# Kernel optimization log

Measured on AMD Instinct MI355X. Metric: run time of the kernel, lower is better.

The kernel has to match this reference:

```python
import jax, jax.numpy as jnp
import numpy as np

N_NODES = 50000
N_EDGES = 800000
IN_CH = 128
HID = 64
OUT_CH = 2
NEG_SLOPE = 0.2


def gcn_conv(x, src, dst, deg_isqrt, W, b):
    # PyG GCNConv: x @ W, symmetric normalization with self-loops, scatter-add, + bias
    h = x @ W  # [N, HID]
    norm = deg_isqrt[src] * deg_isqrt[dst]  # [E+N]
    msg = h[src] * norm[:, None]  # gather + scale
    out = jax.ops.segment_sum(msg, dst, num_segments=x.shape[0])
    return out + b


def setup_inputs() -> dict:
    key = jax.random.key(0)
    ks = jax.random.split(key, 16)
    glorot = lambda k, i, o: jax.random.normal(k, (i, o), jnp.float32) * jnp.sqrt(2.0 / (i + o))
    inp = {
        "node_features": jax.random.normal(ks[0], (N_NODES, IN_CH), jnp.float32),
        "edge_index": jax.random.randint(ks[1], (2, N_EDGES), 0, N_NODES, jnp.int64 if jax.config.jax_enable_x64 else jnp.int32),
        "fc1_W": glorot(ks[2], IN_CH, 32), "fc1_b": jnp.zeros((32,), jnp.float32),
        "fc2_W": glorot(ks[3], 32, HID), "fc2_b": jnp.zeros((HID,), jnp.float32),
        "conv1_W": glorot(ks[4], HID, HID), "conv1_b": jnp.zeros((HID,), jnp.float32),
        "conv2_W": glorot(ks[5], HID, HID), "conv2_b": jnp.zeros((HID,), jnp.float32),
        "conv3_W": glorot(ks[6], HID, HID), "conv3_b": jnp.zeros((HID,), jnp.float32),
        "conv4_W": glorot(ks[7], HID, HID), "conv4_b": jnp.zeros((HID,), jnp.float32),
        "final_W": glorot(ks[8], HID, OUT_CH), "final_b": jnp.zeros((OUT_CH,), jnp.float32),
    }
    return inp


def reference(node_features, edge_index, fc1_W, fc1_b, fc2_W, fc2_b,
              conv1_W, conv1_b, conv2_W, conv2_b, conv3_W, conv3_b,
              conv4_W, conv4_b, final_W, final_b):
    N = node_features.shape[0]
    # add self-loops once (shared by all conv layers)
    loops = jnp.arange(N, dtype=edge_index.dtype)
    src = jnp.concatenate([edge_index[0], loops])
    dst = jnp.concatenate([edge_index[1], loops])
    deg = jax.ops.segment_sum(jnp.ones_like(dst, jnp.float32), dst, num_segments=N)
    deg_isqrt = jnp.where(deg > 0, jax.lax.rsqrt(jnp.maximum(deg, 1.0)), 0.0)

    lrelu = lambda x: jnp.where(x >= 0, x, NEG_SLOPE * x)

    x = jax.nn.relu(node_features @ fc1_W + fc1_b) @ fc2_W + fc2_b  # fc stack
    out1 = lrelu(gcn_conv(x, src, dst, deg_isqrt, conv1_W, conv1_b))
    out2 = lrelu(gcn_conv(out1, src, dst, deg_isqrt, conv2_W, conv2_b)) + out1
    out3 = lrelu(gcn_conv(out2, src, dst, deg_isqrt, conv3_W, conv3_b))
    out4 = gcn_conv(out3, src, dst, deg_isqrt, conv4_W, conv4_b) + out2
    return out4 @ final_W + final_b
```

## Files before the change

### kernel.cpp

```cpp
#include <hip/hip_runtime.h>

#define NN 50000
#define NE 800000

typedef unsigned short u16;
typedef unsigned int u32;

__device__ inline float rlf(float v, int l) {
    return __int_as_float(__builtin_amdgcn_readlane(__float_as_int(v), l));
}
__device__ inline u16 f2bf(float f) {
    u32 u = __float_as_uint(f);
    u32 r = (u + 0x7FFFu + ((u >> 16) & 1u)) >> 16;
    return (u16)r;
}
__device__ inline float lo16(u32 q) { return __uint_as_float(q << 16); }
__device__ inline float hi16(u32 q) { return __uint_as_float(q & 0xffff0000u); }

__global__ void k_hist(const int* __restrict__ dst, int* __restrict__ cnt) {
    int e = blockIdx.x * 256 + threadIdx.x;
    if (e < NE) atomicAdd(&cnt[dst[e]], 1);
}

__global__ void k_disq(const int* __restrict__ cnt, float* __restrict__ disq) {
    int i = blockIdx.x * 256 + threadIdx.x;
    if (i < NN) disq[i] = rsqrtf((float)cnt[i] + 1.0f);
}

__global__ __launch_bounds__(1024) void k_scan(int* __restrict__ cnt,
                                               int* __restrict__ rowptr) {
    __shared__ int wsum[16];
    __shared__ int carry;
    int t = threadIdx.x, wave = t >> 6, lane = t & 63;
    if (t == 0) { carry = 0; rowptr[0] = 0; }
    __syncthreads();
    for (int base = 0; base < NN; base += 1024) {
        int i = base + t;
        int x = (i < NN) ? cnt[i] : 0;
        if (i < NN) cnt[i] = 0;
        for (int off = 1; off < 64; off <<= 1) {
            int y = __shfl_up(x, off, 64);
            if (lane >= off) x += y;
        }
        if (lane == 63) wsum[wave] = x;
        __syncthreads();
        if (wave == 0 && lane < 16) {
            int w = wsum[lane];
            for (int off = 1; off < 16; off <<= 1) {
                int y = __shfl_up(w, off, 16);
                if (lane >= off) w += y;
            }
            wsum[lane] = w;
        }
        __syncthreads();
        int incl = carry + ((wave > 0) ? wsum[wave - 1] : 0) + x;
        if (i < NN) rowptr[i + 1] = incl;
        __syncthreads();
        if (t == 1023) carry = incl;
        __syncthreads();
    }
}

__global__ void k_fill(const int* __restrict__ src, const int* __restrict__ dst,
                       const int* __restrict__ rowptr, int* __restrict__ cur,
                       int* __restrict__ esrc) {
    int e = blockIdx.x * 256 + threadIdx.x;
    if (e < NE) {
        int d = dst[e];
        int pos = rowptr[d] + atomicAdd(&cur[d], 1);
        esrc[pos] = src[e];
    }
}

__global__ __launch_bounds__(64) void k_foldw(
    const float* __restrict__ fc2W, const float* __restrict__ b2,
    const float* __restrict__ c1W, float* __restrict__ W2c,
    float* __restrict__ b2c) {
    int c = threadIdx.x;
    int j = blockIdx.x;
    float s = 0.f;
    if (j < 32) {
        for (int k = 0; k < 64; ++k) s = fmaf(fc2W[j * 64 + k], c1W[k * 64 + c], s);
        W2c[j * 64 + c] = s;
    } else {
        for (int k = 0; k < 64; ++k) s = fmaf(b2[k], c1W[k * 64 + c], s);
        b2c[c] = s;
    }
}

__global__ __launch_bounds__(256) void k_fc(
    const float* __restrict__ nf,
    const float* __restrict__ W1, const float* __restrict__ b1,
    const float* __restrict__ W2c, const float* __restrict__ b2c,
    const float* __restrict__ disq, u16* __restrict__ Hb) {
    int lane = threadIdx.x & 63;
    int c = lane & 31, h = lane >> 5;
    int wid = (blockIdx.x * 256 + threadIdx.x) >> 6;
    int nwaves = (gridDim.x * 256) >> 6;
    float w1[64], w2[32];
    #pragma unroll
    for (int j = 0; j < 64; ++j) w1[j] = W1[(h * 64 + j) * 32 + c];
    #pragma unroll
    for (int j = 0; j < 32; ++j) w2[j] = W2c[j * 64 + lane];
    float b1c = b1[c], b2l = b2c[lane];
    for (int n = wid; n < NN; n += nwaves) {
        float x0 = nf[(size_t)n * 128 + lane];
        float x1 = nf[(size_t)n * 128 + 64 + lane];
        float s = 0.f;
        #pragma unroll
        for (int j = 0; j < 64; ++j) {
            float xa = rlf(x0, j), xb = rlf(x1, j);
            s = fmaf(h ? xb : xa, w1[j], s);
        }
        s += __shfl_xor(s, 32, 64);
        float hv = fmaxf(s + b1c, 0.f);
        float o = b2l;
        #pragma unroll
        for (int j = 0; j < 32; ++j) o = fmaf(rlf(hv, j), w2[j], o);
        Hb[(size_t)n * 64 + lane] = f2bf(disq[n] * o);
    }
}

__global__ __launch_bounds__(256) void k_gemm64(
    const float* __restrict__ X, const float* __restrict__ W,
    const float* __restrict__ disq, u16* __restrict__ Hb) {
    int lane = threadIdx.x & 63;
    int wid = (blockIdx.x * 256 + threadIdx.x) >> 6;
    int nwaves = (gridDim.x * 256) >> 6;
    float wcol[64];
    #pragma unroll
    for (int k = 0; k < 64; ++k) wcol[k] = W[k * 64 + lane];
    for (int n = wid; n < NN; n += nwaves) {
        float xv = X[(size_t)n * 64 + lane];
        float acc = 0.f;
        #pragma unroll
        for (int k = 0; k < 64; ++k) acc = fmaf(rlf(xv, k), wcol[k], acc);
        Hb[(size_t)n * 64 + lane] = f2bf(disq[n] * acc);
    }
}

__global__ __launch_bounds__(256) void k_csr_conv(
    const u16* __restrict__ Hb, const int* __restrict__ rowptr,
    const int* __restrict__ esrc, const float* __restrict__ disq,
    const float* __restrict__ b, const float* __restrict__ res,
    float* __restrict__ out, int do_lrelu) {
    int lane = threadIdx.x & 63;
    int half = lane >> 5;
    int cl = (lane & 31) * 2;
    int n = (blockIdx.x * 256 + threadIdx.x) >> 6;
    if (n >= NN) return;
    int beg = rowptr[n], end = rowptr[n + 1];
    float a0 = 0.f, a1 = 0.f;
    for (int base = beg; base < end; base += 64) {
        int cnt = min(64, end - base);
        int idx = (lane < cnt) ? esrc[base + lane] : 0;
        int j = 0;
        for (; j + 8 <= cnt; j += 8) {
            int p0 = __builtin_amdgcn_readlane(idx, j + 0);
            int p1 = __builtin_amdgcn_readlane(idx, j + 1);
            int p2 = __builtin_amdgcn_readlane(idx, j + 2);
            int p3 = __builtin_amdgcn_readlane(idx, j + 3);
            int p4 = __builtin_amdgcn_readlane(idx, j + 4);
            int p5 = __builtin_amdgcn_readlane(idx, j + 5);
            int p6 = __builtin_amdgcn_readlane(idx, j + 6);
            int p7 = __builtin_amdgcn_readlane(idx, j + 7);
            int sA = half ? p1 : p0;
            int sB = half ? p3 : p2;
            int sC = half ? p5 : p4;
            int sD = half ? p7 : p6;
            u32 qA = *(const u32*)(Hb + ((size_t)sA * 64 + cl));
            u32 qB = *(const u32*)(Hb + ((size_t)sB * 64 + cl));
            u32 qC = *(const u32*)(Hb + ((size_t)sC * 64 + cl));
            u32 qD = *(const u32*)(Hb + ((size_t)sD * 64 + cl));
            a0 += (lo16(qA) + lo16(qB)) + (lo16(qC) + lo16(qD));
            a1 += (hi16(qA) + hi16(qB)) + (hi16(qC) + hi16(qD));
        }
        for (; j + 2 <= cnt; j += 2) {
            int p0 = __builtin_amdgcn_readlane(idx, j);
            int p1 = __builtin_amdgcn_readlane(idx, j + 1);
            int s = half ? p1 : p0;
            u32 q = *(const u32*)(Hb + ((size_t)s * 64 + cl));
            a0 += lo16(q);
            a1 += hi16(q);
        }
        if (j < cnt) {
            int s = __builtin_amdgcn_readlane(idx, j);
            if (!half) {
                u32 q = *(const u32*)(Hb + ((size_t)s * 64 + cl));
                a0 += lo16(q);
                a1 += hi16(q);
            }
        }
    }
    a0 += __shfl_xor(a0, 32, 64);
    a1 += __shfl_xor(a1, 32, 64);
    u32 qs = *(const u32*)(Hb + ((size_t)n * 64 + cl));
    a0 += lo16(qs);
    a1 += hi16(qs);
    float dn = disq[n];
    float v0 = dn * a0 + b[cl];
    float v1 = dn * a1 + b[cl + 1];
    if (do_lrelu) {
        v0 = (v0 >= 0.f) ? v0 : 0.2f * v0;
        v1 = (v1 >= 0.f) ? v1 : 0.2f * v1;
    }
    if (res) {
        float2 r = *(const float2*)(res + ((size_t)n * 64 + cl));
        v0 += r.x;
        v1 += r.y;
    }
    if (!half) {
        float2 o;
        o.x = v0;
        o.y = v1;
        *(float2*)(out + ((size_t)n * 64 + cl)) = o;
    }
}

__global__ __launch_bounds__(256) void k_csr_conv_final(
    const u16* __restrict__ Hb, const int* __restrict__ rowptr,
    const int* __restrict__ esrc, const float* __restrict__ disq,
    const float* __restrict__ b, const float* __restrict__ res,
    const float* __restrict__ FW, const float* __restrict__ fb,
    float* __restrict__ out) {
    int lane = threadIdx.x & 63;
    int half = lane >> 5;
    int cl = (lane & 31) * 2;
    int n = (blockIdx.x * 256 + threadIdx.x) >> 6;
    if (n >= NN) return;
    int beg = rowptr[n], end = rowptr[n + 1];
    float a0 = 0.f, a1 = 0.f;
    for (int base = beg; base < end; base += 64) {
        int cnt = min(64, end - base);
        int idx = (lane < cnt) ? esrc[base + lane] : 0;
        int j = 0;
        for (; j + 8 <= cnt; j += 8) {
            int p0 = __builtin_amdgcn_readlane(idx, j + 0);
            int p1 = __builtin_amdgcn_readlane(idx, j + 1);
            int p2 = __builtin_amdgcn_readlane(idx, j + 2);
            int p3 = __builtin_amdgcn_readlane(idx, j + 3);
            int p4 = __builtin_amdgcn_readlane(idx, j + 4);
            int p5 = __builtin_amdgcn_readlane(idx, j + 5);
            int p6 = __builtin_amdgcn_readlane(idx, j + 6);
            int p7 = __builtin_amdgcn_readlane(idx, j + 7);
            int sA = half ? p1 : p0;
            int sB = half ? p3 : p2;
            int sC = half ? p5 : p4;
            int sD = half ? p7 : p6;
            u32 qA = *(const u32*)(Hb + ((size_t)sA * 64 + cl));
            u32 qB = *(const u32*)(Hb + ((size_t)sB * 64 + cl));
            u32 qC = *(const u32*)(Hb + ((size_t)sC * 64 + cl));
            u32 qD = *(const u32*)(Hb + ((size_t)sD * 64 + cl));
            a0 += (lo16(qA) + lo16(qB)) + (lo16(qC) + lo16(qD));
            a1 += (hi16(qA) + hi16(qB)) + (hi16(qC) + hi16(qD));
        }
        for (; j + 2 <= cnt; j += 2) {
            int p0 = __builtin_amdgcn_readlane(idx, j);
            int p1 = __builtin_amdgcn_readlane(idx, j + 1);
            int s = half ? p1 : p0;
            u32 q = *(const u32*)(Hb + ((size_t)s * 64 + cl));
            a0 += lo16(q);
            a1 += hi16(q);
        }
        if (j < cnt) {
            int s = __builtin_amdgcn_readlane(idx, j);
            if (!half) {
                u32 q = *(const u32*)(Hb + ((size_t)s * 64 + cl));
                a0 += lo16(q);
                a1 += hi16(q);
            }
        }
    }
    a0 += __shfl_xor(a0, 32, 64);
    a1 += __shfl_xor(a1, 32, 64);
    u32 qs = *(const u32*)(Hb + ((size_t)n * 64 + cl));
    a0 += lo16(qs);
    a1 += hi16(qs);
    float dn = disq[n];
    float2 r = *(const float2*)(res + ((size_t)n * 64 + cl));
    float v0 = dn * a0 + b[cl] + r.x;
    float v1 = dn * a1 + b[cl + 1] + r.y;
    float p0 = v0 * FW[cl * 2 + 0] + v1 * FW[(cl + 1) * 2 + 0];
    float p1 = v0 * FW[cl * 2 + 1] + v1 * FW[(cl + 1) * 2 + 1];
    for (int off = 16; off; off >>= 1) {
        p0 += __shfl_xor(p0, off, 64);
        p1 += __shfl_xor(p1, off, 64);
    }
    if (lane == 0) {
        out[n * 2 + 0] = p0 + fb[0];
        out[n * 2 + 1] = p1 + fb[1];
    }
}

extern "C" void kernel_launch(void* const* d_in, const int* in_sizes, int n_in,
                              void* d_out, int out_size, void* d_ws, size_t ws_size,
                              hipStream_t stream) {
    const float* nf   = (const float*)d_in[0];
    const int*   ei   = (const int*)d_in[1];
    const float* fc1W = (const float*)d_in[2];
    const float* fc1b = (const float*)d_in[3];
    const float* fc2W = (const float*)d_in[4];
    const float* fc2b = (const float*)d_in[5];
    const float* cW[4] = {(const float*)d_in[6], (const float*)d_in[8],
                          (const float*)d_in[10], (const float*)d_in[12]};
    const float* cb[4] = {(const float*)d_in[7], (const float*)d_in[9],
                          (const float*)d_in[11], (const float*)d_in[13]};
    const float* fW = (const float*)d_in[14];
    const float* fb = (const float*)d_in[15];
    const int* src = ei;
    const int* dst = ei + NE;

    float* ws     = (float*)d_ws;
    float* disq   = ws;
    int*   cnt    = (int*)(ws + 50048);
    int*   rowptr = cnt + 50048;
    int*   esrc   = rowptr + 50056;
    float* W2c    = (float*)(esrc + 800000);
    float* b2c    = W2c + 2048;
    float* B0     = b2c + 64;
    float* B1     = B0 + (size_t)NN * 64;
    u16*   Hb     = (u16*)(B1 + (size_t)NN * 64);

    hipMemsetAsync(cnt, 0, 50048 * sizeof(int), stream);
    k_hist<<<(NE + 255) / 256, 256, 0, stream>>>(dst, cnt);
    k_disq<<<(NN + 255) / 256, 256, 0, stream>>>(cnt, disq);
    k_scan<<<1, 1024, 0, stream>>>(cnt, rowptr);
    k_fill<<<(NE + 255) / 256, 256, 0, stream>>>(src, dst, rowptr, cnt, esrc);

    k_foldw<<<33, 64, 0, stream>>>(fc2W, fc2b, cW[0], W2c, b2c);
    k_fc<<<1024, 256, 0, stream>>>(nf, fc1W, fc1b, W2c, b2c, disq, Hb);

    const int cgrid = (NN * 64 + 255) / 256;

    k_csr_conv<<<cgrid, 256, 0, stream>>>(Hb, rowptr, esrc, disq, cb[0], nullptr, B1, 1);
    k_gemm64<<<512, 256, 0, stream>>>(B1, cW[1], disq, Hb);
    k_csr_conv<<<cgrid, 256, 0, stream>>>(Hb, rowptr, esrc, disq, cb[1], B1, B0, 1);
    k_gemm64<<<512, 256, 0, stream>>>(B0, cW[2], disq, Hb);
    k_csr_conv<<<cgrid, 256, 0, stream>>>(Hb, rowptr, esrc, disq, cb[2], nullptr, B1, 1);
    k_gemm64<<<512, 256, 0, stream>>>(B1, cW[3], disq, Hb);
    k_csr_conv_final<<<cgrid, 256, 0, stream>>>(Hb, rowptr, esrc, disq, cb[3], B0,
                                                fW, fb, (float*)d_out);
}
```

Before: 356.6 us.

## Fuse preprocessing launches and store CSR source indices as 16-bit

```diff
diff --git a/kernel.cpp b/kernel.cpp
--- a/kernel.cpp
+++ b/kernel.cpp
@@ -2,6 +2,9 @@
 
 #define NN 50000
 #define NE 800000
+#define HIST_BLOCKS ((NE + 255) / 256)
+#define FILL_BLOCKS HIST_BLOCKS
+#define FC_BLOCKS 1024
 
 typedef unsigned short u16;
 typedef unsigned int u32;
@@ -17,18 +20,32 @@
 __device__ inline float lo16(u32 q) { return __uint_as_float(q << 16); }
 __device__ inline float hi16(u32 q) { return __uint_as_float(q & 0xffff0000u); }
 
-__global__ void k_hist(const int* __restrict__ dst, int* __restrict__ cnt) {
-    int e = blockIdx.x * 256 + threadIdx.x;
-    if (e < NE) atomicAdd(&cnt[dst[e]], 1);
-}
-
-__global__ void k_disq(const int* __restrict__ cnt, float* __restrict__ disq) {
-    int i = blockIdx.x * 256 + threadIdx.x;
-    if (i < NN) disq[i] = rsqrtf((float)cnt[i] + 1.0f);
+__global__ __launch_bounds__(256) void k_hist_foldw(
+    const int* __restrict__ dst, int* __restrict__ cnt,
+    const float* __restrict__ fc2W, const float* __restrict__ b2,
+    const float* __restrict__ c1W, float* __restrict__ W2c,
+    float* __restrict__ b2c) {
+    if (blockIdx.x < HIST_BLOCKS) {
+        int e = blockIdx.x * 256 + threadIdx.x;
+        if (e < NE) atomicAdd(&cnt[dst[e]], 1);
+    } else {
+        int j = (blockIdx.x - HIST_BLOCKS) * 4 + (threadIdx.x >> 6);
+        int c = threadIdx.x & 63;
+        if (j < 32) {
+            float s = 0.f;
+            for (int k = 0; k < 64; ++k) s = fmaf(fc2W[j * 64 + k], c1W[k * 64 + c], s);
+            W2c[j * 64 + c] = s;
+        } else if (j == 32) {
+            float s = 0.f;
+            for (int k = 0; k < 64; ++k) s = fmaf(b2[k], c1W[k * 64 + c], s);
+            b2c[c] = s;
+        }
+    }
 }
 
 __global__ __launch_bounds__(1024) void k_scan(int* __restrict__ cnt,
-                                               int* __restrict__ rowptr) {
+                                               int* __restrict__ rowptr,
+                                               float* __restrict__ disq) {
     __shared__ int wsum[16];
     __shared__ int carry;
     int t = threadIdx.x, wave = t >> 6, lane = t & 63;
@@ -37,7 +54,10 @@
     for (int base = 0; base < NN; base += 1024) {
         int i = base + t;
         int x = (i < NN) ? cnt[i] : 0;
-        if (i < NN) cnt[i] = 0;
+        if (i < NN) {
+            cnt[i] = 0;
+            disq[i] = rsqrtf((float)x + 1.0f);
+        }
         for (int off = 1; off < 64; off <<= 1) {
             int y = __shfl_up(x, off, 64);
             if (lane >= off) x += y;
@@ -61,42 +81,27 @@
     }
 }
 
-__global__ void k_fill(const int* __restrict__ src, const int* __restrict__ dst,
-                       const int* __restrict__ rowptr, int* __restrict__ cur,
-                       int* __restrict__ esrc) {
-    int e = blockIdx.x * 256 + threadIdx.x;
-    if (e < NE) {
-        int d = dst[e];
-        int pos = rowptr[d] + atomicAdd(&cur[d], 1);
-        esrc[pos] = src[e];
-    }
-}
-
-__global__ __launch_bounds__(64) void k_foldw(
-    const float* __restrict__ fc2W, const float* __restrict__ b2,
-    const float* __restrict__ c1W, float* __restrict__ W2c,
-    float* __restrict__ b2c) {
-    int c = threadIdx.x;
-    int j = blockIdx.x;
-    float s = 0.f;
-    if (j < 32) {
-        for (int k = 0; k < 64; ++k) s = fmaf(fc2W[j * 64 + k], c1W[k * 64 + c], s);
-        W2c[j * 64 + c] = s;
-    } else {
-        for (int k = 0; k < 64; ++k) s = fmaf(b2[k], c1W[k * 64 + c], s);
-        b2c[c] = s;
-    }
-}
-
-__global__ __launch_bounds__(256) void k_fc(
+__global__ __launch_bounds__(256) void k_fill_fc(
+    const int* __restrict__ src, const int* __restrict__ dst,
+    const int* __restrict__ rowptr, int* __restrict__ cur,
+    u16* __restrict__ esrc,
     const float* __restrict__ nf,
     const float* __restrict__ W1, const float* __restrict__ b1,
     const float* __restrict__ W2c, const float* __restrict__ b2c,
     const float* __restrict__ disq, u16* __restrict__ Hb) {
+    if (blockIdx.x < FILL_BLOCKS) {
+        int e = blockIdx.x * 256 + threadIdx.x;
+        if (e < NE) {
+            int d = dst[e];
+            int pos = rowptr[d] + atomicAdd(&cur[d], 1);
+            esrc[pos] = (u16)src[e];
+        }
+        return;
+    }
     int lane = threadIdx.x & 63;
     int c = lane & 31, h = lane >> 5;
-    int wid = (blockIdx.x * 256 + threadIdx.x) >> 6;
-    int nwaves = (gridDim.x * 256) >> 6;
+    int wid = ((blockIdx.x - FILL_BLOCKS) * 256 + threadIdx.x) >> 6;
+    int nwaves = (FC_BLOCKS * 256) >> 6;
     float w1[64], w2[32];
     #pragma unroll
     for (int j = 0; j < 64; ++j) w1[j] = W1[(h * 64 + j) * 32 + c];
@@ -141,7 +146,7 @@
 
 __global__ __launch_bounds__(256) void k_csr_conv(
     const u16* __restrict__ Hb, const int* __restrict__ rowptr,
-    const int* __restrict__ esrc, const float* __restrict__ disq,
+    const u16* __restrict__ esrc, const float* __restrict__ disq,
     const float* __restrict__ b, const float* __restrict__ res,
     float* __restrict__ out, int do_lrelu) {
     int lane = threadIdx.x & 63;
@@ -153,7 +158,7 @@
     float a0 = 0.f, a1 = 0.f;
     for (int base = beg; base < end; base += 64) {
         int cnt = min(64, end - base);
-        int idx = (lane < cnt) ? esrc[base + lane] : 0;
+        int idx = (lane < cnt) ? (int)esrc[base + lane] : 0;
         int j = 0;
         for (; j + 8 <= cnt; j += 8) {
             int p0 = __builtin_amdgcn_readlane(idx, j + 0);
@@ -219,7 +224,7 @@
 
 __global__ __launch_bounds__(256) void k_csr_conv_final(
     const u16* __restrict__ Hb, const int* __restrict__ rowptr,
-    const int* __restrict__ esrc, const float* __restrict__ disq,
+    const u16* __restrict__ esrc, const float* __restrict__ disq,
     const float* __restrict__ b, const float* __restrict__ res,
     const float* __restrict__ FW, const float* __restrict__ fb,
     float* __restrict__ out) {
@@ -232,7 +237,7 @@
     float a0 = 0.f, a1 = 0.f;
     for (int base = beg; base < end; base += 64) {
         int cnt = min(64, end - base);
-        int idx = (lane < cnt) ? esrc[base + lane] : 0;
+        int idx = (lane < cnt) ? (int)esrc[base + lane] : 0;
         int j = 0;
         for (; j + 8 <= cnt; j += 8) {
             int p0 = __builtin_amdgcn_readlane(idx, j + 0);
@@ -314,7 +319,7 @@
     float* disq   = ws;
     int*   cnt    = (int*)(ws + 50048);
     int*   rowptr = cnt + 50048;
-    int*   esrc   = rowptr + 50056;
+    u16*   esrc   = (u16*)(rowptr + 50056);
     float* W2c    = (float*)(esrc + 800000);
     float* b2c    = W2c + 2048;
     float* B0     = b2c + 64;
@@ -322,13 +327,11 @@
     u16*   Hb     = (u16*)(B1 + (size_t)NN * 64);
 
     hipMemsetAsync(cnt, 0, 50048 * sizeof(int), stream);
-    k_hist<<<(NE + 255) / 256, 256, 0, stream>>>(dst, cnt);
-    k_disq<<<(NN + 255) / 256, 256, 0, stream>>>(cnt, disq);
-    k_scan<<<1, 1024, 0, stream>>>(cnt, rowptr);
-    k_fill<<<(NE + 255) / 256, 256, 0, stream>>>(src, dst, rowptr, cnt, esrc);
-
-    k_foldw<<<33, 64, 0, stream>>>(fc2W, fc2b, cW[0], W2c, b2c);
-    k_fc<<<1024, 256, 0, stream>>>(nf, fc1W, fc1b, W2c, b2c, disq, Hb);
+    k_hist_foldw<<<HIST_BLOCKS + 9, 256, 0, stream>>>(dst, cnt, fc2W, fc2b, cW[0],
+                                                      W2c, b2c);
+    k_scan<<<1, 1024, 0, stream>>>(cnt, rowptr, disq);
+    k_fill_fc<<<FILL_BLOCKS + FC_BLOCKS, 256, 0, stream>>>(
+        src, dst, rowptr, cnt, esrc, nf, fc1W, fc1b, W2c, b2c, disq, Hb);
 
     const int cgrid = (NN * 64 + 255) / 256;
 
```

Result: no change. 353.4 us (-0.9%).
